# Performance work log

Measured on AMD Instinct MI355X. Metric: run time of the kernel, lower is better.

Reference implementation:

```python
import jax, jax.numpy as jnp
import numpy as np

U = I = 4096; E = 128; K = 4; D = E // K; R = 3; B = 512; L = 100
LAMB = 0.5; L2NORM = 1e-4; EPS = 1e-8


def _l2norm(x, axis):
    n = jnp.sqrt(jnp.sum(x * x, axis=axis, keepdims=True))
    return x / jnp.maximum(n, 1e-12)


def setup_inputs() -> dict:
    key = jax.random.key(0)
    ks = jax.random.split(key, 16)
    def adj(k, shape, p=0.01):
        return jax.random.bernoulli(k, p, shape).astype(jnp.float32)
    relation_mats = adj(ks[0], (R, U, I))
    item_graphs = adj(ks[1], (R, I, I))
    train_matrix = relation_mats[0]
    inp = {
        "user": jax.random.randint(ks[2], (B, 1), 0, U),
        "item": jax.random.randint(ks[3], (B, L), 0, I),
        "user_embedding": jax.random.normal(ks[4], (U, E), jnp.float32) * 0.1,
        "item_embedding": jax.random.normal(ks[5], (I, E), jnp.float32) * 0.1,
        "mgnn_weight": jax.random.normal(ks[6], (R,), jnp.float32),
        "item_behaviour_W": jax.random.normal(ks[7], (R, E, E), jnp.float32) * 0.05,
        "item_propagate_W": jax.random.normal(ks[8], (R, E, E), jnp.float32) * 0.05,
        "W": jax.random.normal(ks[9], (E, E), jnp.float32) * 0.05,
        "W_K": jax.random.normal(ks[10], (K, D, E), jnp.float32) * 0.05,
        "B_K": jax.random.normal(ks[11], (K, D), jnp.float32) * 0.05,
        "train_matrix": train_matrix,
        "relation_mats": relation_mats,
        "item_graphs": item_graphs,
        "item_graph_degree": item_graphs.sum(axis=2, keepdims=True),  # [R,I,1]
        "user_behaviour_degree": relation_mats.sum(axis=2).T,  # [U,R]
    }
    return inp


def reference(user, item, user_embedding, item_embedding, mgnn_weight,
              item_behaviour_W, item_propagate_W, W, W_K, B_K,
              train_matrix, relation_mats, item_graphs, item_graph_degree,
              user_behaviour_degree):
    # behaviour weighting: [U,R]
    total_weight = user_behaviour_degree @ mgnn_weight[:, None]  # [U,1]
    ubw = user_behaviour_degree * mgnn_weight[None, :] / (total_weight + EPS)

    # K-head projections (relation-independent; original recomputes identically per relation)
    s_i = _l2norm(jax.nn.relu(jnp.einsum('kde,ie->kdi', W_K, item_embedding) + B_K[..., None]), axis=1)  # [K,D,I]
    s_u0 = _l2norm(jax.nn.relu(jnp.einsum('kde,ue->kdu', W_K, user_embedding) + B_K[..., None]), axis=1)  # [K,D,U]
    s_u0 = jnp.transpose(s_u0, (2, 0, 1))  # [U,K,D]

    ue_blocks = user_embedding.reshape(U, K, D)
    logits = jnp.einsum('ukd,kdi->kui', ue_blocks, s_i)  # [K,U,I]
    r = jax.nn.softmax(logits, axis=0)  # exp / sum over K heads

    user_feature = jnp.zeros((U, E), user_embedding.dtype)
    score2 = jnp.zeros((B, L), user_embedding.dtype)
    for i in range(R):
        rel = relation_mats[i]  # [U,I]
        # item-item propagation
        tip = ((item_graphs[i] @ item_embedding) / (item_graph_degree[i] + EPS)) @ item_propagate_W[i]  # [I,E]
        tmp_item_emb = tip[item]  # [B,L,E]
        # attention-weighted user-item propagation per head
        s_u = s_u0 + jnp.einsum('kui,kdi->ukd', r * rel[None], s_i)  # [U,K,D]
        tun = _l2norm(s_u, axis=2).reshape(U, E)  # tmp_user_neighbour
        tuinp = (rel @ tip) / (user_behaviour_degree[:, i:i + 1] + EPS)  # [U,E]
        user_feature = user_feature + ubw[:, i:i + 1] * tun
        proj = tuinp @ item_behaviour_W[i]  # [U,E]
        score2 = score2 + jnp.sum(proj[user[:, 0]][:, None, :] * tmp_item_emb, axis=2)
    score2 = score2 / R

    item_feature = (train_matrix.T @ user_embedding) @ W  # [I,E]
    user_feature = user_feature @ W  # [U,E]

    uf = user_feature[user[:, 0]][:, None, :]  # [B,1,E]
    itf = item_feature[item]  # [B,L,E]
    score1 = jnp.sum(uf * itf, axis=2)  # [B,L]
    scores = score1 + LAMB * score2
    L2_loss = L2NORM * (L * jnp.sum(uf ** 2) + jnp.sum(itf ** 2))
    return scores, L2_loss
```

## Files before the change

### kernel.cpp

```cpp
#include <hip/hip_runtime.h>

#define NU 4096
#define NI 4096
#define NR 3
#define NB 512
#define NL 100
#define FEPS 1e-8f

#define WS_SI    0
#define WS_EMBW  524288
#define WS_TIP   2097152
#define WS_UEW   3670016
#define WS_ITEMF 4194304
#define WS_WTUN  4718592
#define WS_PROJ  4915200
#define WS_UF    5111808
#define WS_UF2P  5177344
#define WS_ITF2P 5177856
#define WS_BMT   5190656

__global__ void k_bmm_si(const float* __restrict__ iemb, const float* __restrict__ ipW,
                         const float* __restrict__ uemb, const float* __restrict__ Wm,
                         const float* __restrict__ WK, const float* __restrict__ BK,
                         float* __restrict__ embW, float* __restrict__ uew,
                         float* __restrict__ si) {
  __shared__ __align__(16) float shbuf[2048];
  int t = threadIdx.x;
  int bid = blockIdx.x;
  if (bid < 1024) {
    int batch = bid >> 8, rb = bid & 255;
    const float* in;
    const float* Wp;
    float* out;
    if (batch < 3) {
      in = iemb;
      Wp = ipW + (size_t)batch * 16384;
      out = embW + (size_t)batch * NI * 128;
    } else {
      in = uemb; Wp = Wm; out = uew;
    }
    const float4* in4 = (const float4*)(in + (size_t)rb * 2048);
    for (int c = t; c < 512; c += 256) ((float4*)shbuf)[c] = in4[c];
    __syncthreads();
    int c = t & 127, g = t >> 7;
    float acc[8];
#pragma unroll
    for (int rr = 0; rr < 8; ++rr) acc[rr] = 0.f;
    for (int e = 0; e < 128; ++e) {
      float wv = Wp[e * 128 + c];
#pragma unroll
      for (int rr = 0; rr < 8; ++rr) acc[rr] += shbuf[(g * 8 + rr) * 128 + e] * wv;
    }
#pragma unroll
    for (int rr = 0; rr < 8; ++rr) out[((size_t)rb * 16 + g * 8 + rr) * 128 + c] = acc[rr];
  } else {
    int tl = t & 127, half = t >> 7;
    int item = (bid - 1024) * 2 + half;
    float* embs = shbuf + half * 128;
    if (tl < 32) ((float4*)embs)[tl] = ((const float4*)(iemb + (size_t)item * 128))[tl];
    __syncthreads();
    float acc = BK[tl];
    const float4* wk4 = (const float4*)(WK + (size_t)tl * 128);
    const float4* e4 = (const float4*)embs;
#pragma unroll 8
    for (int c = 0; c < 32; ++c) {
      float4 w = wk4[c], v = e4[c];
      acc += w.x * v.x + w.y * v.y + w.z * v.z + w.w * v.w;
    }
    acc = fmaxf(acc, 0.f);
    float sq = acc * acc;
#pragma unroll
    for (int m = 1; m <= 16; m <<= 1) sq += __shfl_xor(sq, m);
    si[(size_t)item * 128 + tl] = acc / fmaxf(sqrtf(sq), 1e-12f);
  }
}

__global__ void k_scan(const float* __restrict__ tm, const float* __restrict__ G,
                       const float* __restrict__ deg, const float* __restrict__ embW,
                       unsigned long long* __restrict__ bmT, float* __restrict__ tip) {
  int bid = blockIdx.x;
  int t = threadIdx.x;
  if (bid < NU) {
    __shared__ unsigned char nib[4][256];
    const float4* r4 = (const float4*)(tm + (size_t)bid * NI);
#pragma unroll
    for (int q = 0; q < 4; ++q) {
      float4 v = r4[q * 256 + t];
      unsigned m = 0;
      if (v.x != 0.f) m |= 1u;
      if (v.y != 0.f) m |= 2u;
      if (v.z != 0.f) m |= 4u;
      if (v.w != 0.f) m |= 8u;
      nib[q][t] = (unsigned char)m;
    }
    __syncthreads();
    if (t < 64) {
      unsigned long long mm = 0;
#pragma unroll
      for (int j = 0; j < 16; ++j) {
        int e = t * 16 + j;
        mm |= (unsigned long long)nib[e >> 8][e & 255] << (4 * j);
      }
      bmT[(size_t)t * NU + bid] = mm;
    }
  } else {
    int gid = bid - NU;
    int r = gid >> 12;
    const float4* row4 = (const float4*)(G + (size_t)gid * NI);
    __shared__ int nz[512];
    __shared__ int cnt;
    __shared__ float4 red[8][32];
    if (t == 0) cnt = 0;
    __syncthreads();
#pragma unroll
    for (int c = 0; c < 4; ++c) {
      int idx4 = c * 256 + t;
      float4 v = row4[idx4];
      int j0 = idx4 << 2;
      if (v.x != 0.f) nz[atomicAdd(&cnt, 1)] = j0;
      if (v.y != 0.f) nz[atomicAdd(&cnt, 1)] = j0 + 1;
      if (v.z != 0.f) nz[atomicAdd(&cnt, 1)] = j0 + 2;
      if (v.w != 0.f) nz[atomicAdd(&cnt, 1)] = j0 + 3;
    }
    __syncthreads();
    int n = min(cnt, 512);
    int g = t >> 5, f = t & 31;
    float4 acc = {0.f, 0.f, 0.f, 0.f};
    const float4* e4 = (const float4*)(embW + (size_t)r * NI * 128);
    for (int p = g; p < n; p += 8) {
      float4 v = e4[(size_t)nz[p] * 32 + f];
      acc.x += v.x; acc.y += v.y; acc.z += v.z; acc.w += v.w;
    }
    red[g][f] = acc;
    __syncthreads();
    if (t < 32) {
      float4 s = red[0][t];
#pragma unroll
      for (int q = 1; q < 8; ++q) {
        float4 v = red[q][t];
        s.x += v.x; s.y += v.y; s.z += v.z; s.w += v.w;
      }
      float inv = 1.f / (deg[gid] + FEPS);
      s.x *= inv; s.y *= inv; s.z *= inv; s.w *= inv;
      ((float4*)(tip + (size_t)gid * 128))[t] = s;
    }
  }
}

__global__ void k_itemf_csc(const unsigned long long* __restrict__ bmT,
                            const float* __restrict__ uew, float* __restrict__ itemf) {
  int i = blockIdx.x;
  int ct = i >> 6;
  unsigned long long bitm = 1ull << (i & 63);
  __shared__ int lst[192];
  __shared__ int cnt;
  __shared__ float red[3][128];
  int t = threadIdx.x;
  if (t == 0) cnt = 0;
  __syncthreads();
  const unsigned long long* col = bmT + (size_t)ct * NU;
#pragma unroll
  for (int cc = 0; cc < 16; ++cc) {
    unsigned long long m = col[cc * 256 + t];
    if (m & bitm) lst[atomicAdd(&cnt, 1)] = cc * 256 + t;
  }
  __syncthreads();
  int n = min(cnt, 192);
  int w = t >> 6, l = t & 63;
  float ax = 0.f, ay = 0.f;
  const float2* uew2 = (const float2*)uew;
  for (int p = w; p < n; p += 4) {
    float2 v = uew2[(size_t)lst[p] * 64 + l];
    ax += v.x; ay += v.y;
  }
  if (w > 0) { red[w - 1][2 * l] = ax; red[w - 1][2 * l + 1] = ay; }
  __syncthreads();
  if (w == 0) {
    float2 o;
    o.x = ax + red[0][2 * l] + red[1][2 * l] + red[2][2 * l];
    o.y = ay + red[0][2 * l + 1] + red[1][2 * l + 1] + red[2][2 * l + 1];
    ((float2*)(itemf + (size_t)i * 128))[l] = o;
  }
}

__global__ void k_user(const int* __restrict__ user, const float* __restrict__ relm,
                       const float* __restrict__ si, const float* __restrict__ tip,
                       const float* __restrict__ uemb, const float* __restrict__ WK,
                       const float* __restrict__ BK, const float* __restrict__ ibW,
                       const float* __restrict__ ubd, const float* __restrict__ mw,
                       float* __restrict__ wtun, float* __restrict__ proj) {
  int bid = blockIdx.x;
  int r = bid >> 9, b = bid & 511;
  int u = user[b];
  const float* rel = relm + ((size_t)r * NU + u) * NI;
  __shared__ int nz[512];
  __shared__ int cnt;
  __shared__ __align__(16) float uel[128];
  __shared__ float redA[4][128];
  __shared__ float redB[4][128];
  __shared__ float tu[128];
  int t = threadIdx.x;
  if (t == 0) cnt = 0;
  if (t < 32) ((float4*)uel)[t] = ((const float4*)(uemb + (size_t)u * 128))[t];
  __syncthreads();
  const float4* rel4 = (const float4*)rel;
#pragma unroll
  for (int c = 0; c < 4; ++c) {
    int idx4 = c * 256 + t;
    float4 v = rel4[idx4];
    int j0 = idx4 << 2;
    if (v.x != 0.f) nz[atomicAdd(&cnt, 1)] = j0;
    if (v.y != 0.f) nz[atomicAdd(&cnt, 1)] = j0 + 1;
    if (v.z != 0.f) nz[atomicAdd(&cnt, 1)] = j0 + 2;
    if (v.w != 0.f) nz[atomicAdd(&cnt, 1)] = j0 + 3;
  }
  __syncthreads();
  int n = min(cnt, 512);
  int wid = t >> 6, lane = t & 63;
  int k = lane >> 4;
  float2 myue = ((const float2*)uel)[lane];
  float sux = 0.f, suy = 0.f, tpx = 0.f, tpy = 0.f;
  const float2* si2 = (const float2*)si;
  const float2* tip2 = (const float2*)(tip + (size_t)r * NI * 128);
  for (int p = wid; p < n; p += 4) {
    int i = nz[p];
    float2 sv = si2[(size_t)i * 64 + lane];
    float lg = myue.x * sv.x + myue.y * sv.y;
    lg += __shfl_xor(lg, 1);
    lg += __shfl_xor(lg, 2);
    lg += __shfl_xor(lg, 4);
    lg += __shfl_xor(lg, 8);
    float l0 = __shfl(lg, 0), l1 = __shfl(lg, 16), l2 = __shfl(lg, 32), l3 = __shfl(lg, 48);
    float mx = fmaxf(fmaxf(l0, l1), fmaxf(l2, l3));
    float e0 = __expf(l0 - mx), e1 = __expf(l1 - mx), e2 = __expf(l2 - mx), e3 = __expf(l3 - mx);
    float inv = 1.f / (e0 + e1 + e2 + e3);
    float myr = (k == 0 ? e0 : k == 1 ? e1 : k == 2 ? e2 : e3) * inv;
    sux += myr * sv.x;
    suy += myr * sv.y;
    float2 tv = tip2[(size_t)i * 64 + lane];
    tpx += tv.x;
    tpy += tv.y;
  }
  redA[wid][2 * lane] = sux; redA[wid][2 * lane + 1] = suy;
  redB[wid][2 * lane] = tpx; redB[wid][2 * lane + 1] = tpy;
  __syncthreads();
  if (t < 128) {
    float suv = redA[0][t] + redA[1][t] + redA[2][t] + redA[3][t];
    float tipv = redB[0][t] + redB[1][t] + redB[2][t] + redB[3][t];
    float a = BK[t];
    const float4* wk4 = (const float4*)(WK + (size_t)t * 128);
    const float4* ue4 = (const float4*)uel;
#pragma unroll 8
    for (int c = 0; c < 32; ++c) {
      float4 w = wk4[c], v = ue4[c];
      a += w.x * v.x + w.y * v.y + w.z * v.z + w.w * v.w;
    }
    a = fmaxf(a, 0.f);
    float sq = a * a;
#pragma unroll
    for (int m = 1; m <= 16; m <<= 1) sq += __shfl_xor(sq, m);
    float su = a / fmaxf(sqrtf(sq), 1e-12f) + suv;
    float sq2 = su * su;
#pragma unroll
    for (int m = 1; m <= 16; m <<= 1) sq2 += __shfl_xor(sq2, m);
    float tun = su / fmaxf(sqrtf(sq2), 1e-12f);
    float d0 = ubd[u * 3], d1 = ubd[u * 3 + 1], d2 = ubd[u * 3 + 2];
    float w0 = mw[0], w1 = mw[1], w2 = mw[2];
    float tw = d0 * w0 + d1 * w1 + d2 * w2;
    float dr = (r == 0 ? d0 : r == 1 ? d1 : d2);
    float wr = (r == 0 ? w0 : r == 1 ? w1 : w2);
    wtun[(size_t)(b * 3 + r) * 128 + t] = (dr * wr / (tw + FEPS)) * tun;
    tu[t] = tipv / (dr + FEPS);
  }
  __syncthreads();
  int ep = t & 127, hh = t >> 7;
  const float* Wb = ibW + (size_t)r * 16384;
  float pacc = 0.f;
  for (int e = hh * 64; e < hh * 64 + 64; ++e) pacc += tu[e] * Wb[e * 128 + ep];
  redA[hh][ep] = pacc;
  __syncthreads();
  if (hh == 0) proj[(size_t)(b * 3 + r) * 128 + ep] = redA[0][ep] + redA[1][ep];
}

__global__ void k_uf(const float* __restrict__ wtun, const float* __restrict__ Wm,
                     float* __restrict__ uf, float* __restrict__ uf2p) {
  int b = blockIdx.x, t = threadIdx.x;
  __shared__ float comb[128];
  __shared__ float part[2];
  comb[t] = wtun[(size_t)(b * 3) * 128 + t] + wtun[(size_t)(b * 3 + 1) * 128 + t] +
            wtun[(size_t)(b * 3 + 2) * 128 + t];
  __syncthreads();
  float acc = 0.f;
  for (int e = 0; e < 128; ++e) acc += comb[e] * Wm[e * 128 + t];
  uf[(size_t)b * 128 + t] = acc;
  float sq = acc * acc;
#pragma unroll
  for (int m = 1; m <= 32; m <<= 1) sq += __shfl_xor(sq, m);
  if ((t & 63) == 0) part[t >> 6] = sq;
  __syncthreads();
  if (t == 0) uf2p[b] = part[0] + part[1];
}

__global__ void k_score(const int* __restrict__ item, const float* __restrict__ itemf,
                        const float* __restrict__ uf, const float* __restrict__ tip,
                        const float* __restrict__ proj, float* __restrict__ out,
                        float* __restrict__ itf2p) {
  int t = threadIdx.x, wid = t >> 6, lane = t & 63;
  int idx = blockIdx.x * 4 + wid;
  int b = idx / NL;
  int it = item[idx];
  float2 av = ((const float2*)(itemf + (size_t)it * 128))[lane];
  float2 cv = ((const float2*)(uf + (size_t)b * 128))[lane];
  float s1 = av.x * cv.x + av.y * cv.y;
  float sqi = av.x * av.x + av.y * av.y;
  float s2 = 0.f;
#pragma unroll
  for (int r = 0; r < 3; ++r) {
    float2 tv = ((const float2*)(tip + ((size_t)r * NI + it) * 128))[lane];
    float2 pv = ((const float2*)(proj + (size_t)(b * 3 + r) * 128))[lane];
    s2 += tv.x * pv.x + tv.y * pv.y;
  }
#pragma unroll
  for (int m = 1; m <= 32; m <<= 1) {
    s1 += __shfl_xor(s1, m);
    s2 += __shfl_xor(s2, m);
    sqi += __shfl_xor(sqi, m);
  }
  if (lane == 0) out[idx] = s1 + 0.5f * (s2 * (1.f / 3.f));
  __shared__ float sh[4];
  if (lane == 0) sh[wid] = sqi;
  __syncthreads();
  if (t == 0) itf2p[blockIdx.x] = sh[0] + sh[1] + sh[2] + sh[3];
}

__global__ void k_final(const float* __restrict__ itf2p, const float* __restrict__ uf2p,
                        float* __restrict__ out) {
  int t = threadIdx.x;
  float v = 0.f;
  for (int i = t; i < 12800; i += 256) v += itf2p[i];
  float vu = 0.f;
  for (int i = t; i < NB; i += 256) vu += uf2p[i];
  v += 100.f * vu;
#pragma unroll
  for (int m = 1; m <= 32; m <<= 1) v += __shfl_xor(v, m);
  __shared__ float sh[4];
  if ((t & 63) == 0) sh[t >> 6] = v;
  __syncthreads();
  if (t == 0) out[NB * NL] = 1e-4f * (sh[0] + sh[1] + sh[2] + sh[3]);
}

extern "C" void kernel_launch(void* const* d_in, const int* in_sizes, int n_in,
                              void* d_out, int out_size, void* d_ws, size_t ws_size,
                              hipStream_t stream) {
  (void)in_sizes; (void)n_in; (void)out_size; (void)ws_size;
  const int* user = (const int*)d_in[0];
  const int* item = (const int*)d_in[1];
  const float* uemb = (const float*)d_in[2];
  const float* iemb = (const float*)d_in[3];
  const float* mw = (const float*)d_in[4];
  const float* ibW = (const float*)d_in[5];
  const float* ipW = (const float*)d_in[6];
  const float* Wm = (const float*)d_in[7];
  const float* WK = (const float*)d_in[8];
  const float* BK = (const float*)d_in[9];
  const float* tm = (const float*)d_in[10];
  const float* relm = (const float*)d_in[11];
  const float* ig = (const float*)d_in[12];
  const float* igd = (const float*)d_in[13];
  const float* ubd = (const float*)d_in[14];
  float* out = (float*)d_out;
  float* ws = (float*)d_ws;
  unsigned long long* bmT = (unsigned long long*)(ws + WS_BMT);

  k_bmm_si<<<3072, 256, 0, stream>>>(iemb, ipW, uemb, Wm, WK, BK,
                                     ws + WS_EMBW, ws + WS_UEW, ws + WS_SI);
  k_scan<<<NU + NR * NI, 256, 0, stream>>>(tm, ig, igd, ws + WS_EMBW, bmT, ws + WS_TIP);
  k_itemf_csc<<<NI, 256, 0, stream>>>(bmT, ws + WS_UEW, ws + WS_ITEMF);
  k_user<<<NR * NB, 256, 0, stream>>>(user, relm, ws + WS_SI, ws + WS_TIP, uemb, WK, BK,
                                      ibW, ubd, mw, ws + WS_WTUN, ws + WS_PROJ);
  k_uf<<<NB, 128, 0, stream>>>(ws + WS_WTUN, Wm, ws + WS_UF, ws + WS_UF2P);
  k_score<<<12800, 256, 0, stream>>>(item, ws + WS_ITEMF, ws + WS_UF, ws + WS_TIP,
                                     ws + WS_PROJ, out, ws + WS_ITF2P);
  k_final<<<1, 256, 0, stream>>>(ws + WS_ITF2P, ws + WS_UF2P, out);
}
```

Before: 186.6 us.

## Bitpack item graphs in streaming kernel and merge sparse gathers into one launch

The dense item-graph rows are now bit-packed in the same kernel as the train-matrix bitmask and the small matmuls, so the dense scan no longer depends on the embW matmul finishing first. A second kernel decodes the bitmasks with ffs to build the neighbour lists, then runs both the tip gather and the itemf column gather. This cuts three launches to two and lets the dense-read phase overlap the matmul blocks. The cost is an extra bitmask buffer write and read, plus a serial ffs loop for 64 threads.

```diff
diff --git a/kernel.cpp b/kernel.cpp
--- a/kernel.cpp
+++ b/kernel.cpp
@@ -18,17 +18,48 @@
 #define WS_UF2P  5177344
 #define WS_ITF2P 5177856
 #define WS_BMT   5190656
-
-__global__ void k_bmm_si(const float* __restrict__ iemb, const float* __restrict__ ipW,
+#define WS_GBITS 5714944
+
+__global__ void k_stream(const float* __restrict__ iemb, const float* __restrict__ ipW,
                          const float* __restrict__ uemb, const float* __restrict__ Wm,
                          const float* __restrict__ WK, const float* __restrict__ BK,
+                         const float* __restrict__ tm, const float* __restrict__ G,
                          float* __restrict__ embW, float* __restrict__ uew,
-                         float* __restrict__ si) {
-  __shared__ __align__(16) float shbuf[2048];
+                         float* __restrict__ si,
+                         unsigned long long* __restrict__ bmT,
+                         unsigned long long* __restrict__ gbits) {
   int t = threadIdx.x;
   int bid = blockIdx.x;
-  if (bid < 1024) {
-    int batch = bid >> 8, rb = bid & 255;
+  if (bid < 16384) {
+    __shared__ unsigned char nib[4][256];
+    const float* src = (bid < NU) ? (tm + (size_t)bid * NI)
+                                  : (G + (size_t)(bid - NU) * NI);
+    const float4* r4 = (const float4*)src;
+#pragma unroll
+    for (int q = 0; q < 4; ++q) {
+      float4 v = r4[q * 256 + t];
+      unsigned m = 0;
+      if (v.x != 0.f) m |= 1u;
+      if (v.y != 0.f) m |= 2u;
+      if (v.z != 0.f) m |= 4u;
+      if (v.w != 0.f) m |= 8u;
+      nib[q][t] = (unsigned char)m;
+    }
+    __syncthreads();
+    if (t < 64) {
+      unsigned long long mm = 0;
+#pragma unroll
+      for (int j = 0; j < 16; ++j) {
+        int e = t * 16 + j;
+        mm |= (unsigned long long)nib[e >> 8][e & 255] << (4 * j);
+      }
+      if (bid < NU) bmT[(size_t)t * NU + bid] = mm;
+      else gbits[(size_t)(bid - NU) * 64 + t] = mm;
+    }
+  } else if (bid < 17408) {
+    __shared__ __align__(16) float shbuf[2048];
+    int lb = bid - 16384;
+    int batch = lb >> 8, rb = lb & 255;
     const float* in;
     const float* Wp;
     float* out;
@@ -54,9 +85,10 @@
 #pragma unroll
     for (int rr = 0; rr < 8; ++rr) out[((size_t)rb * 16 + g * 8 + rr) * 128 + c] = acc[rr];
   } else {
+    __shared__ __align__(16) float embs2[256];
     int tl = t & 127, half = t >> 7;
-    int item = (bid - 1024) * 2 + half;
-    float* embs = shbuf + half * 128;
+    int item = (bid - 17408) * 2 + half;
+    float* embs = embs2 + half * 128;
     if (tl < 32) ((float4*)embs)[tl] = ((const float4*)(iemb + (size_t)item * 128))[tl];
     __syncthreads();
     float acc = BK[tl];
@@ -75,52 +107,28 @@
   }
 }
 
-__global__ void k_scan(const float* __restrict__ tm, const float* __restrict__ G,
-                       const float* __restrict__ deg, const float* __restrict__ embW,
-                       unsigned long long* __restrict__ bmT, float* __restrict__ tip) {
+__global__ void k_gather(const unsigned long long* __restrict__ gbits,
+                         const unsigned long long* __restrict__ bmT,
+                         const float* __restrict__ embW, const float* __restrict__ uew,
+                         const float* __restrict__ deg,
+                         float* __restrict__ tip, float* __restrict__ itemf) {
+  int t = threadIdx.x;
   int bid = blockIdx.x;
-  int t = threadIdx.x;
-  if (bid < NU) {
-    __shared__ unsigned char nib[4][256];
-    const float4* r4 = (const float4*)(tm + (size_t)bid * NI);
-#pragma unroll
-    for (int q = 0; q < 4; ++q) {
-      float4 v = r4[q * 256 + t];
-      unsigned m = 0;
-      if (v.x != 0.f) m |= 1u;
-      if (v.y != 0.f) m |= 2u;
-      if (v.z != 0.f) m |= 4u;
-      if (v.w != 0.f) m |= 8u;
-      nib[q][t] = (unsigned char)m;
-    }
-    __syncthreads();
-    if (t < 64) {
-      unsigned long long mm = 0;
-#pragma unroll
-      for (int j = 0; j < 16; ++j) {
-        int e = t * 16 + j;
-        mm |= (unsigned long long)nib[e >> 8][e & 255] << (4 * j);
-      }
-      bmT[(size_t)t * NU + bid] = mm;
-    }
-  } else {
-    int gid = bid - NU;
-    int r = gid >> 12;
-    const float4* row4 = (const float4*)(G + (size_t)gid * NI);
+  if (bid < 12288) {
+    int r = bid >> 12;
     __shared__ int nz[512];
     __shared__ int cnt;
     __shared__ float4 red[8][32];
     if (t == 0) cnt = 0;
     __syncthreads();
-#pragma unroll
-    for (int c = 0; c < 4; ++c) {
-      int idx4 = c * 256 + t;
-      float4 v = row4[idx4];
-      int j0 = idx4 << 2;
-      if (v.x != 0.f) nz[atomicAdd(&cnt, 1)] = j0;
-      if (v.y != 0.f) nz[atomicAdd(&cnt, 1)] = j0 + 1;
-      if (v.z != 0.f) nz[atomicAdd(&cnt, 1)] = j0 + 2;
-      if (v.w != 0.f) nz[atomicAdd(&cnt, 1)] = j0 + 3;
+    if (t < 64) {
+      unsigned long long m = gbits[(size_t)bid * 64 + t];
+      int base = t * 64;
+      while (m) {
+        int b = __ffsll(m) - 1;
+        m &= m - 1;
+        nz[atomicAdd(&cnt, 1)] = base + b;
+      }
     }
     __syncthreads();
     int n = min(cnt, 512);
@@ -140,46 +148,42 @@
         float4 v = red[q][t];
         s.x += v.x; s.y += v.y; s.z += v.z; s.w += v.w;
       }
-      float inv = 1.f / (deg[gid] + FEPS);
+      float inv = 1.f / (deg[bid] + FEPS);
       s.x *= inv; s.y *= inv; s.z *= inv; s.w *= inv;
-      ((float4*)(tip + (size_t)gid * 128))[t] = s;
-    }
-  }
-}
-
-__global__ void k_itemf_csc(const unsigned long long* __restrict__ bmT,
-                            const float* __restrict__ uew, float* __restrict__ itemf) {
-  int i = blockIdx.x;
-  int ct = i >> 6;
-  unsigned long long bitm = 1ull << (i & 63);
-  __shared__ int lst[192];
-  __shared__ int cnt;
-  __shared__ float red[3][128];
-  int t = threadIdx.x;
-  if (t == 0) cnt = 0;
-  __syncthreads();
-  const unsigned long long* col = bmT + (size_t)ct * NU;
-#pragma unroll
-  for (int cc = 0; cc < 16; ++cc) {
-    unsigned long long m = col[cc * 256 + t];
-    if (m & bitm) lst[atomicAdd(&cnt, 1)] = cc * 256 + t;
-  }
-  __syncthreads();
-  int n = min(cnt, 192);
-  int w = t >> 6, l = t & 63;
-  float ax = 0.f, ay = 0.f;
-  const float2* uew2 = (const float2*)uew;
-  for (int p = w; p < n; p += 4) {
-    float2 v = uew2[(size_t)lst[p] * 64 + l];
-    ax += v.x; ay += v.y;
-  }
-  if (w > 0) { red[w - 1][2 * l] = ax; red[w - 1][2 * l + 1] = ay; }
-  __syncthreads();
-  if (w == 0) {
-    float2 o;
-    o.x = ax + red[0][2 * l] + red[1][2 * l] + red[2][2 * l];
-    o.y = ay + red[0][2 * l + 1] + red[1][2 * l + 1] + red[2][2 * l + 1];
-    ((float2*)(itemf + (size_t)i * 128))[l] = o;
+      ((float4*)(tip + (size_t)bid * 128))[t] = s;
+    }
+  } else {
+    int i = bid - 12288;
+    int ct = i >> 6;
+    unsigned long long bitm = 1ull << (i & 63);
+    __shared__ int lst[192];
+    __shared__ int cnt2;
+    __shared__ float red2[3][128];
+    if (t == 0) cnt2 = 0;
+    __syncthreads();
+    const unsigned long long* col = bmT + (size_t)ct * NU;
+#pragma unroll
+    for (int cc = 0; cc < 16; ++cc) {
+      unsigned long long m = col[cc * 256 + t];
+      if (m & bitm) lst[atomicAdd(&cnt2, 1)] = cc * 256 + t;
+    }
+    __syncthreads();
+    int n = min(cnt2, 192);
+    int w = t >> 6, l = t & 63;
+    float ax = 0.f, ay = 0.f;
+    const float2* uew2 = (const float2*)uew;
+    for (int p = w; p < n; p += 4) {
+      float2 v = uew2[(size_t)lst[p] * 64 + l];
+      ax += v.x; ay += v.y;
+    }
+    if (w > 0) { red2[w - 1][2 * l] = ax; red2[w - 1][2 * l + 1] = ay; }
+    __syncthreads();
+    if (w == 0) {
+      float2 o;
+      o.x = ax + red2[0][2 * l] + red2[1][2 * l] + red2[2][2 * l];
+      o.y = ay + red2[0][2 * l + 1] + red2[1][2 * l + 1] + red2[2][2 * l + 1];
+      ((float2*)(itemf + (size_t)i * 128))[l] = o;
+    }
   }
 }
 
@@ -371,11 +375,12 @@
   float* out = (float*)d_out;
   float* ws = (float*)d_ws;
   unsigned long long* bmT = (unsigned long long*)(ws + WS_BMT);
-
-  k_bmm_si<<<3072, 256, 0, stream>>>(iemb, ipW, uemb, Wm, WK, BK,
-                                     ws + WS_EMBW, ws + WS_UEW, ws + WS_SI);
-  k_scan<<<NU + NR * NI, 256, 0, stream>>>(tm, ig, igd, ws + WS_EMBW, bmT, ws + WS_TIP);
-  k_itemf_csc<<<NI, 256, 0, stream>>>(bmT, ws + WS_UEW, ws + WS_ITEMF);
+  unsigned long long* gbits = (unsigned long long*)(ws + WS_GBITS);
+
+  k_stream<<<19456, 256, 0, stream>>>(iemb, ipW, uemb, Wm, WK, BK, tm, ig,
+                                      ws + WS_EMBW, ws + WS_UEW, ws + WS_SI, bmT, gbits);
+  k_gather<<<16384, 256, 0, stream>>>(gbits, bmT, ws + WS_EMBW, ws + WS_UEW, igd,
+                                      ws + WS_TIP, ws + WS_ITEMF);
   k_user<<<NR * NB, 256, 0, stream>>>(user, relm, ws + WS_SI, ws + WS_TIP, uemb, WK, BK,
                                       ibW, ubd, mw, ws + WS_WTUN, ws + WS_PROJ);
   k_uf<<<NB, 128, 0, stream>>>(ws + WS_WTUN, Wm, ws + WS_UF, ws + WS_UF2P);
```

After: 189.0 us. About the same (+1.3%).

## Regroup kernels by dependency to merge independent stages into shared launches

Applied to the files above, without the earlier changes.

Moves the train-matrix bitmap scan into the first launch alongside the embedding GEMMs and s_i projection, leaving k_scan to handle only the item-graph propagation. Fuses the item-feature CSC gather and the per-user attention kernel into one launch, since both depend only on earlier stages. This drops one kernel launch and lets independent work share the GPU instead of running serially. The trade-off is larger combined shared-memory footprints per block and mixed block types that may lower occupancy.

```diff
diff --git a/kernel.cpp b/kernel.cpp
--- a/kernel.cpp
+++ b/kernel.cpp
@@ -19,68 +19,15 @@
 #define WS_ITF2P 5177856
 #define WS_BMT   5190656
 
-__global__ void k_bmm_si(const float* __restrict__ iemb, const float* __restrict__ ipW,
-                         const float* __restrict__ uemb, const float* __restrict__ Wm,
-                         const float* __restrict__ WK, const float* __restrict__ BK,
-                         float* __restrict__ embW, float* __restrict__ uew,
-                         float* __restrict__ si) {
-  __shared__ __align__(16) float shbuf[2048];
+__global__ void k_prep(const float* __restrict__ iemb, const float* __restrict__ ipW,
+                       const float* __restrict__ uemb, const float* __restrict__ Wm,
+                       const float* __restrict__ WK, const float* __restrict__ BK,
+                       const float* __restrict__ tm,
+                       float* __restrict__ embW, float* __restrict__ uew,
+                       float* __restrict__ si, unsigned long long* __restrict__ bmT) {
   int t = threadIdx.x;
   int bid = blockIdx.x;
-  if (bid < 1024) {
-    int batch = bid >> 8, rb = bid & 255;
-    const float* in;
-    const float* Wp;
-    float* out;
-    if (batch < 3) {
-      in = iemb;
-      Wp = ipW + (size_t)batch * 16384;
-      out = embW + (size_t)batch * NI * 128;
-    } else {
-      in = uemb; Wp = Wm; out = uew;
-    }
-    const float4* in4 = (const float4*)(in + (size_t)rb * 2048);
-    for (int c = t; c < 512; c += 256) ((float4*)shbuf)[c] = in4[c];
-    __syncthreads();
-    int c = t & 127, g = t >> 7;
-    float acc[8];
-#pragma unroll
-    for (int rr = 0; rr < 8; ++rr) acc[rr] = 0.f;
-    for (int e = 0; e < 128; ++e) {
-      float wv = Wp[e * 128 + c];
-#pragma unroll
-      for (int rr = 0; rr < 8; ++rr) acc[rr] += shbuf[(g * 8 + rr) * 128 + e] * wv;
-    }
-#pragma unroll
-    for (int rr = 0; rr < 8; ++rr) out[((size_t)rb * 16 + g * 8 + rr) * 128 + c] = acc[rr];
-  } else {
-    int tl = t & 127, half = t >> 7;
-    int item = (bid - 1024) * 2 + half;
-    float* embs = shbuf + half * 128;
-    if (tl < 32) ((float4*)embs)[tl] = ((const float4*)(iemb + (size_t)item * 128))[tl];
-    __syncthreads();
-    float acc = BK[tl];
-    const float4* wk4 = (const float4*)(WK + (size_t)tl * 128);
-    const float4* e4 = (const float4*)embs;
-#pragma unroll 8
-    for (int c = 0; c < 32; ++c) {
-      float4 w = wk4[c], v = e4[c];
-      acc += w.x * v.x + w.y * v.y + w.z * v.z + w.w * v.w;
-    }
-    acc = fmaxf(acc, 0.f);
-    float sq = acc * acc;
-#pragma unroll
-    for (int m = 1; m <= 16; m <<= 1) sq += __shfl_xor(sq, m);
-    si[(size_t)item * 128 + tl] = acc / fmaxf(sqrtf(sq), 1e-12f);
-  }
-}
-
-__global__ void k_scan(const float* __restrict__ tm, const float* __restrict__ G,
-                       const float* __restrict__ deg, const float* __restrict__ embW,
-                       unsigned long long* __restrict__ bmT, float* __restrict__ tip) {
-  int bid = blockIdx.x;
-  int t = threadIdx.x;
-  if (bid < NU) {
+  if (bid < 4096) {
     __shared__ unsigned char nib[4][256];
     const float4* r4 = (const float4*)(tm + (size_t)bid * NI);
 #pragma unroll
@@ -103,19 +50,163 @@
       }
       bmT[(size_t)t * NU + bid] = mm;
     }
+  } else if (bid < 5120) {
+    __shared__ __align__(16) float shbuf[2048];
+    int lb = bid - 4096;
+    int batch = lb >> 8, rb = lb & 255;
+    const float* in;
+    const float* Wp;
+    float* outp;
+    if (batch < 3) {
+      in = iemb;
+      Wp = ipW + (size_t)batch * 16384;
+      outp = embW + (size_t)batch * NI * 128;
+    } else {
+      in = uemb; Wp = Wm; outp = uew;
+    }
+    const float4* in4 = (const float4*)(in + (size_t)rb * 2048);
+    for (int c = t; c < 512; c += 256) ((float4*)shbuf)[c] = in4[c];
+    __syncthreads();
+    int c = t & 127, g = t >> 7;
+    float acc[8];
+#pragma unroll
+    for (int rr = 0; rr < 8; ++rr) acc[rr] = 0.f;
+    for (int e = 0; e < 128; ++e) {
+      float wv = Wp[e * 128 + c];
+#pragma unroll
+      for (int rr = 0; rr < 8; ++rr) acc[rr] += shbuf[(g * 8 + rr) * 128 + e] * wv;
+    }
+#pragma unroll
+    for (int rr = 0; rr < 8; ++rr) outp[((size_t)rb * 16 + g * 8 + rr) * 128 + c] = acc[rr];
   } else {
-    int gid = bid - NU;
-    int r = gid >> 12;
-    const float4* row4 = (const float4*)(G + (size_t)gid * NI);
+    __shared__ __align__(16) float embs2[256];
+    int tl = t & 127, half = t >> 7;
+    int item = (bid - 5120) * 2 + half;
+    float* embs = embs2 + half * 128;
+    if (tl < 32) ((float4*)embs)[tl] = ((const float4*)(iemb + (size_t)item * 128))[tl];
+    __syncthreads();
+    float acc = BK[tl];
+    const float4* wk4 = (const float4*)(WK + (size_t)tl * 128);
+    const float4* e4 = (const float4*)embs;
+#pragma unroll 8
+    for (int cc = 0; cc < 32; ++cc) {
+      float4 w = wk4[cc], v = e4[cc];
+      acc += w.x * v.x + w.y * v.y + w.z * v.z + w.w * v.w;
+    }
+    acc = fmaxf(acc, 0.f);
+    float sq = acc * acc;
+#pragma unroll
+    for (int m = 1; m <= 16; m <<= 1) sq += __shfl_xor(sq, m);
+    si[(size_t)item * 128 + tl] = acc / fmaxf(sqrtf(sq), 1e-12f);
+  }
+}
+
+__global__ void k_scan(const float* __restrict__ G, const float* __restrict__ deg,
+                       const float* __restrict__ embW, float* __restrict__ tip) {
+  int gid = blockIdx.x;
+  int t = threadIdx.x;
+  int r = gid >> 12;
+  const float4* row4 = (const float4*)(G + (size_t)gid * NI);
+  __shared__ int nz[512];
+  __shared__ int cnt;
+  __shared__ float4 red[8][32];
+  if (t == 0) cnt = 0;
+  __syncthreads();
+#pragma unroll
+  for (int c = 0; c < 4; ++c) {
+    int idx4 = c * 256 + t;
+    float4 v = row4[idx4];
+    int j0 = idx4 << 2;
+    if (v.x != 0.f) nz[atomicAdd(&cnt, 1)] = j0;
+    if (v.y != 0.f) nz[atomicAdd(&cnt, 1)] = j0 + 1;
+    if (v.z != 0.f) nz[atomicAdd(&cnt, 1)] = j0 + 2;
+    if (v.w != 0.f) nz[atomicAdd(&cnt, 1)] = j0 + 3;
+  }
+  __syncthreads();
+  int n = min(cnt, 512);
+  int g = t >> 5, f = t & 31;
+  float4 acc = {0.f, 0.f, 0.f, 0.f};
+  const float4* e4 = (const float4*)(embW + (size_t)r * NI * 128);
+  for (int p = g; p < n; p += 8) {
+    float4 v = e4[(size_t)nz[p] * 32 + f];
+    acc.x += v.x; acc.y += v.y; acc.z += v.z; acc.w += v.w;
+  }
+  red[g][f] = acc;
+  __syncthreads();
+  if (t < 32) {
+    float4 s = red[0][t];
+#pragma unroll
+    for (int q = 1; q < 8; ++q) {
+      float4 v = red[q][t];
+      s.x += v.x; s.y += v.y; s.z += v.z; s.w += v.w;
+    }
+    float inv = 1.f / (deg[gid] + FEPS);
+    s.x *= inv; s.y *= inv; s.z *= inv; s.w *= inv;
+    ((float4*)(tip + (size_t)gid * 128))[t] = s;
+  }
+}
+
+__global__ void k_mid(const unsigned long long* __restrict__ bmT,
+                      const float* __restrict__ uew, float* __restrict__ itemf,
+                      const int* __restrict__ user, const float* __restrict__ relm,
+                      const float* __restrict__ si, const float* __restrict__ tip,
+                      const float* __restrict__ uemb, const float* __restrict__ WK,
+                      const float* __restrict__ BK, const float* __restrict__ ibW,
+                      const float* __restrict__ ubd, const float* __restrict__ mw,
+                      float* __restrict__ wtun, float* __restrict__ proj) {
+  int t = threadIdx.x;
+  int bid = blockIdx.x;
+  if (bid < 4096) {
+    int i = bid;
+    int ct = i >> 6;
+    unsigned long long bitm = 1ull << (i & 63);
+    __shared__ int lst[192];
+    __shared__ int cnt2;
+    __shared__ float red2[3][128];
+    if (t == 0) cnt2 = 0;
+    __syncthreads();
+    const unsigned long long* col = bmT + (size_t)ct * NU;
+#pragma unroll
+    for (int cc = 0; cc < 16; ++cc) {
+      unsigned long long m = col[cc * 256 + t];
+      if (m & bitm) lst[atomicAdd(&cnt2, 1)] = cc * 256 + t;
+    }
+    __syncthreads();
+    int n = min(cnt2, 192);
+    int w = t >> 6, l = t & 63;
+    float ax = 0.f, ay = 0.f;
+    const float2* uew2 = (const float2*)uew;
+    for (int p = w; p < n; p += 4) {
+      float2 v = uew2[(size_t)lst[p] * 64 + l];
+      ax += v.x; ay += v.y;
+    }
+    if (w > 0) { red2[w - 1][2 * l] = ax; red2[w - 1][2 * l + 1] = ay; }
+    __syncthreads();
+    if (w == 0) {
+      float2 o;
+      o.x = ax + red2[0][2 * l] + red2[1][2 * l] + red2[2][2 * l];
+      o.y = ay + red2[0][2 * l + 1] + red2[1][2 * l + 1] + red2[2][2 * l + 1];
+      ((float2*)(itemf + (size_t)i * 128))[l] = o;
+    }
+  } else {
+    int ub = bid - 4096;
+    int r = ub >> 9, b = ub & 511;
+    int u = user[b];
+    const float* rel = relm + ((size_t)r * NU + u) * NI;
     __shared__ int nz[512];
     __shared__ int cnt;
-    __shared__ float4 red[8][32];
+    __shared__ __align__(16) float uel[128];
+    __shared__ float redA[4][128];
+    __shared__ float redB[4][128];
+    __shared__ float tu[128];
     if (t == 0) cnt = 0;
-    __syncthreads();
+    if (t < 32) ((float4*)uel)[t] = ((const float4*)(uemb + (size_t)u * 128))[t];
+    __syncthreads();
+    const float4* rel4 = (const float4*)rel;
 #pragma unroll
     for (int c = 0; c < 4; ++c) {
       int idx4 = c * 256 + t;
-      float4 v = row4[idx4];
+      float4 v = rel4[idx4];
       int j0 = idx4 << 2;
       if (v.x != 0.f) nz[atomicAdd(&cnt, 1)] = j0;
       if (v.y != 0.f) nz[atomicAdd(&cnt, 1)] = j0 + 1;
@@ -124,162 +215,71 @@
     }
     __syncthreads();
     int n = min(cnt, 512);
-    int g = t >> 5, f = t & 31;
-    float4 acc = {0.f, 0.f, 0.f, 0.f};
-    const float4* e4 = (const float4*)(embW + (size_t)r * NI * 128);
-    for (int p = g; p < n; p += 8) {
-      float4 v = e4[(size_t)nz[p] * 32 + f];
-      acc.x += v.x; acc.y += v.y; acc.z += v.z; acc.w += v.w;
-    }
-    red[g][f] = acc;
-    __syncthreads();
-    if (t < 32) {
-      float4 s = red[0][t];
-#pragma unroll
-      for (int q = 1; q < 8; ++q) {
-        float4 v = red[q][t];
-        s.x += v.x; s.y += v.y; s.z += v.z; s.w += v.w;
+    int wid = t >> 6, lane = t & 63;
+    int k = lane >> 4;
+    float2 myue = ((const float2*)uel)[lane];
+    float sux = 0.f, suy = 0.f, tpx = 0.f, tpy = 0.f;
+    const float2* si2 = (const float2*)si;
+    const float2* tip2 = (const float2*)(tip + (size_t)r * NI * 128);
+    for (int p = wid; p < n; p += 4) {
+      int i = nz[p];
+      float2 sv = si2[(size_t)i * 64 + lane];
+      float lg = myue.x * sv.x + myue.y * sv.y;
+      lg += __shfl_xor(lg, 1);
+      lg += __shfl_xor(lg, 2);
+      lg += __shfl_xor(lg, 4);
+      lg += __shfl_xor(lg, 8);
+      float l0 = __shfl(lg, 0), l1 = __shfl(lg, 16), l2 = __shfl(lg, 32), l3 = __shfl(lg, 48);
+      float mx = fmaxf(fmaxf(l0, l1), fmaxf(l2, l3));
+      float e0 = __expf(l0 - mx), e1 = __expf(l1 - mx), e2 = __expf(l2 - mx), e3 = __expf(l3 - mx);
+      float inv = 1.f / (e0 + e1 + e2 + e3);
+      float myr = (k == 0 ? e0 : k == 1 ? e1 : k == 2 ? e2 : e3) * inv;
+      sux += myr * sv.x;
+      suy += myr * sv.y;
+      float2 tv = tip2[(size_t)i * 64 + lane];
+      tpx += tv.x;
+      tpy += tv.y;
+    }
+    redA[wid][2 * lane] = sux; redA[wid][2 * lane + 1] = suy;
+    redB[wid][2 * lane] = tpx; redB[wid][2 * lane + 1] = tpy;
+    __syncthreads();
+    if (t < 128) {
+      float suv = redA[0][t] + redA[1][t] + redA[2][t] + redA[3][t];
+      float tipv = redB[0][t] + redB[1][t] + redB[2][t] + redB[3][t];
+      float a = BK[t];
+      const float4* wk4 = (const float4*)(WK + (size_t)t * 128);
+      const float4* ue4 = (const float4*)uel;
+#pragma unroll 8
+      for (int c = 0; c < 32; ++c) {
+        float4 w = wk4[c], v = ue4[c];
+        a += w.x * v.x + w.y * v.y + w.z * v.z + w.w * v.w;
       }
-      float inv = 1.f / (deg[gid] + FEPS);
-      s.x *= inv; s.y *= inv; s.z *= inv; s.w *= inv;
-      ((float4*)(tip + (size_t)gid * 128))[t] = s;
-    }
-  }
-}
-
-__global__ void k_itemf_csc(const unsigned long long* __restrict__ bmT,
-                            const float* __restrict__ uew, float* __restrict__ itemf) {
-  int i = blockIdx.x;
-  int ct = i >> 6;
-  unsigned long long bitm = 1ull << (i & 63);
-  __shared__ int lst[192];
-  __shared__ int cnt;
-  __shared__ float red[3][128];
-  int t = threadIdx.x;
-  if (t == 0) cnt = 0;
-  __syncthreads();
-  const unsigned long long* col = bmT + (size_t)ct * NU;
-#pragma unroll
-  for (int cc = 0; cc < 16; ++cc) {
-    unsigned long long m = col[cc * 256 + t];
-    if (m & bitm) lst[atomicAdd(&cnt, 1)] = cc * 256 + t;
-  }
-  __syncthreads();
-  int n = min(cnt, 192);
-  int w = t >> 6, l = t & 63;
-  float ax = 0.f, ay = 0.f;
-  const float2* uew2 = (const float2*)uew;
-  for (int p = w; p < n; p += 4) {
-    float2 v = uew2[(size_t)lst[p] * 64 + l];
-    ax += v.x; ay += v.y;
-  }
-  if (w > 0) { red[w - 1][2 * l] = ax; red[w - 1][2 * l + 1] = ay; }
-  __syncthreads();
-  if (w == 0) {
-    float2 o;
-    o.x = ax + red[0][2 * l] + red[1][2 * l] + red[2][2 * l];
-    o.y = ay + red[0][2 * l + 1] + red[1][2 * l + 1] + red[2][2 * l + 1];
-    ((float2*)(itemf + (size_t)i * 128))[l] = o;
-  }
-}
-
-__global__ void k_user(const int* __restrict__ user, const float* __restrict__ relm,
-                       const float* __restrict__ si, const float* __restrict__ tip,
-                       const float* __restrict__ uemb, const float* __restrict__ WK,
-                       const float* __restrict__ BK, const float* __restrict__ ibW,
-                       const float* __restrict__ ubd, const float* __restrict__ mw,
-                       float* __restrict__ wtun, float* __restrict__ proj) {
-  int bid = blockIdx.x;
-  int r = bid >> 9, b = bid & 511;
-  int u = user[b];
-  const float* rel = relm + ((size_t)r * NU + u) * NI;
-  __shared__ int nz[512];
-  __shared__ int cnt;
-  __shared__ __align__(16) float uel[128];
-  __shared__ float redA[4][128];
-  __shared__ float redB[4][128];
-  __shared__ float tu[128];
-  int t = threadIdx.x;
-  if (t == 0) cnt = 0;
-  if (t < 32) ((float4*)uel)[t] = ((const float4*)(uemb + (size_t)u * 128))[t];
-  __syncthreads();
-  const float4* rel4 = (const float4*)rel;
-#pragma unroll
-  for (int c = 0; c < 4; ++c) {
-    int idx4 = c * 256 + t;
-    float4 v = rel4[idx4];
-    int j0 = idx4 << 2;
-    if (v.x != 0.f) nz[atomicAdd(&cnt, 1)] = j0;
-    if (v.y != 0.f) nz[atomicAdd(&cnt, 1)] = j0 + 1;
-    if (v.z != 0.f) nz[atomicAdd(&cnt, 1)] = j0 + 2;
-    if (v.w != 0.f) nz[atomicAdd(&cnt, 1)] = j0 + 3;
-  }
-  __syncthreads();
-  int n = min(cnt, 512);
-  int wid = t >> 6, lane = t & 63;
-  int k = lane >> 4;
-  float2 myue = ((const float2*)uel)[lane];
-  float sux = 0.f, suy = 0.f, tpx = 0.f, tpy = 0.f;
-  const float2* si2 = (const float2*)si;
-  const float2* tip2 = (const float2*)(tip + (size_t)r * NI * 128);
-  for (int p = wid; p < n; p += 4) {
-    int i = nz[p];
-    float2 sv = si2[(size_t)i * 64 + lane];
-    float lg = myue.x * sv.x + myue.y * sv.y;
-    lg += __shfl_xor(lg, 1);
-    lg += __shfl_xor(lg, 2);
-    lg += __shfl_xor(lg, 4);
-    lg += __shfl_xor(lg, 8);
-    float l0 = __shfl(lg, 0), l1 = __shfl(lg, 16), l2 = __shfl(lg, 32), l3 = __shfl(lg, 48);
-    float mx = fmaxf(fmaxf(l0, l1), fmaxf(l2, l3));
-    float e0 = __expf(l0 - mx), e1 = __expf(l1 - mx), e2 = __expf(l2 - mx), e3 = __expf(l3 - mx);
-    float inv = 1.f / (e0 + e1 + e2 + e3);
-    float myr = (k == 0 ? e0 : k == 1 ? e1 : k == 2 ? e2 : e3) * inv;
-    sux += myr * sv.x;
-    suy += myr * sv.y;
-    float2 tv = tip2[(size_t)i * 64 + lane];
-    tpx += tv.x;
-    tpy += tv.y;
-  }
-  redA[wid][2 * lane] = sux; redA[wid][2 * lane + 1] = suy;
-  redB[wid][2 * lane] = tpx; redB[wid][2 * lane + 1] = tpy;
-  __syncthreads();
-  if (t < 128) {
-    float suv = redA[0][t] + redA[1][t] + redA[2][t] + redA[3][t];
-    float tipv = redB[0][t] + redB[1][t] + redB[2][t] + redB[3][t];
-    float a = BK[t];
-    const float4* wk4 = (const float4*)(WK + (size_t)t * 128);
-    const float4* ue4 = (const float4*)uel;
-#pragma unroll 8
-    for (int c = 0; c < 32; ++c) {
-      float4 w = wk4[c], v = ue4[c];
-      a += w.x * v.x + w.y * v.y + w.z * v.z + w.w * v.w;
-    }
-    a = fmaxf(a, 0.f);
-    float sq = a * a;
-#pragma unroll
-    for (int m = 1; m <= 16; m <<= 1) sq += __shfl_xor(sq, m);
-    float su = a / fmaxf(sqrtf(sq), 1e-12f) + suv;
-    float sq2 = su * su;
-#pragma unroll
-    for (int m = 1; m <= 16; m <<= 1) sq2 += __shfl_xor(sq2, m);
-    float tun = su / fmaxf(sqrtf(sq2), 1e-12f);
-    float d0 = ubd[u * 3], d1 = ubd[u * 3 + 1], d2 = ubd[u * 3 + 2];
-    float w0 = mw[0], w1 = mw[1], w2 = mw[2];
-    float tw = d0 * w0 + d1 * w1 + d2 * w2;
-    float dr = (r == 0 ? d0 : r == 1 ? d1 : d2);
-    float wr = (r == 0 ? w0 : r == 1 ? w1 : w2);
-    wtun[(size_t)(b * 3 + r) * 128 + t] = (dr * wr / (tw + FEPS)) * tun;
-    tu[t] = tipv / (dr + FEPS);
-  }
-  __syncthreads();
-  int ep = t & 127, hh = t >> 7;
-  const float* Wb = ibW + (size_t)r * 16384;
-  float pacc = 0.f;
-  for (int e = hh * 64; e < hh * 64 + 64; ++e) pacc += tu[e] * Wb[e * 128 + ep];
-  redA[hh][ep] = pacc;
-  __syncthreads();
-  if (hh == 0) proj[(size_t)(b * 3 + r) * 128 + ep] = redA[0][ep] + redA[1][ep];
+      a = fmaxf(a, 0.f);
+      float sq = a * a;
+#pragma unroll
+      for (int m = 1; m <= 16; m <<= 1) sq += __shfl_xor(sq, m);
+      float su = a / fmaxf(sqrtf(sq), 1e-12f) + suv;
+      float sq2 = su * su;
+#pragma unroll
+      for (int m = 1; m <= 16; m <<= 1) sq2 += __shfl_xor(sq2, m);
+      float tun = su / fmaxf(sqrtf(sq2), 1e-12f);
+      float d0 = ubd[u * 3], d1 = ubd[u * 3 + 1], d2 = ubd[u * 3 + 2];
+      float w0 = mw[0], w1 = mw[1], w2 = mw[2];
+      float tw = d0 * w0 + d1 * w1 + d2 * w2;
+      float dr = (r == 0 ? d0 : r == 1 ? d1 : d2);
+      float wr = (r == 0 ? w0 : r == 1 ? w1 : w2);
+      wtun[(size_t)(b * 3 + r) * 128 + t] = (dr * wr / (tw + FEPS)) * tun;
+      tu[t] = tipv / (dr + FEPS);
+    }
+    __syncthreads();
+    int ep = t & 127, hh = t >> 7;
+    const float* Wb = ibW + (size_t)r * 16384;
+    float pacc = 0.f;
+    for (int e = hh * 64; e < hh * 64 + 64; ++e) pacc += tu[e] * Wb[e * 128 + ep];
+    redA[hh][ep] = pacc;
+    __syncthreads();
+    if (hh == 0) proj[(size_t)(b * 3 + r) * 128 + ep] = redA[0][ep] + redA[1][ep];
+  }
 }
 
 __global__ void k_uf(const float* __restrict__ wtun, const float* __restrict__ Wm,
@@ -372,12 +372,12 @@
   float* ws = (float*)d_ws;
   unsigned long long* bmT = (unsigned long long*)(ws + WS_BMT);
 
-  k_bmm_si<<<3072, 256, 0, stream>>>(iemb, ipW, uemb, Wm, WK, BK,
-                                     ws + WS_EMBW, ws + WS_UEW, ws + WS_SI);
-  k_scan<<<NU + NR * NI, 256, 0, stream>>>(tm, ig, igd, ws + WS_EMBW, bmT, ws + WS_TIP);
-  k_itemf_csc<<<NI, 256, 0, stream>>>(bmT, ws + WS_UEW, ws + WS_ITEMF);
-  k_user<<<NR * NB, 256, 0, stream>>>(user, relm, ws + WS_SI, ws + WS_TIP, uemb, WK, BK,
-                                      ibW, ubd, mw, ws + WS_WTUN, ws + WS_PROJ);
+  k_prep<<<7168, 256, 0, stream>>>(iemb, ipW, uemb, Wm, WK, BK, tm,
+                                   ws + WS_EMBW, ws + WS_UEW, ws + WS_SI, bmT);
+  k_scan<<<NR * NI, 256, 0, stream>>>(ig, igd, ws + WS_EMBW, ws + WS_TIP);
+  k_mid<<<5632, 256, 0, stream>>>(bmT, ws + WS_UEW, ws + WS_ITEMF, user, relm,
+                                  ws + WS_SI, ws + WS_TIP, uemb, WK, BK, ibW,
+                                  ubd, mw, ws + WS_WTUN, ws + WS_PROJ);
   k_uf<<<NB, 128, 0, stream>>>(ws + WS_WTUN, Wm, ws + WS_UF, ws + WS_UF2P);
   k_score<<<12800, 256, 0, stream>>>(item, ws + WS_ITEMF, ws + WS_UF, ws + WS_TIP,
                                      ws + WS_PROJ, out, ws + WS_ITF2P);
```

New measurement: 191.4 us. 1.03x slower.
